# Kernel tuning notes

Measured on AMD Instinct MI355X. Metric: run time of the kernel, lower is better.

## Reference

```python
import jax, jax.numpy as jnp
from jax import lax
import numpy as np
from itertools import permutations, combinations

GRID = (8, 8, 8)  # width, height, depth


def _build_complex(size):
    """Freudenthal (Kuhn) triangulation of the 3D voxel grid.

    Equivalent role to scipy Delaunay on the regular grid (which is degenerate
    anyway): 6 tetrahedra per unit cube, plus all unique faces, edges, verts.
    Returns:
      simp_verts [n,4] int32 : vertex ids of each simplex, padded by repetition
      simp_dim   [n]   int32 : simplex dimension 0..3
      bnd_cof, bnd_face [m] int32 : (cofacet_id, face_id) boundary incidences
    """
    W, H, D = size

    def vid(p):
        return (p[..., 0] * H + p[..., 1]) * D + p[..., 2]

    e = np.eye(3, dtype=np.int64)
    gx, gy, gz = np.meshgrid(np.arange(W - 1), np.arange(H - 1), np.arange(D - 1), indexing="ij")
    base = np.stack([gx, gy, gz], -1).reshape(-1, 3)
    tet_list = []
    for p in permutations(range(3)):
        v0 = base
        v1 = v0 + e[p[0]]
        v2 = v1 + e[p[1]]
        v3 = v2 + e[p[2]]
        tet_list.append(np.stack([vid(v0), vid(v1), vid(v2), vid(v3)], -1))
    tets = np.unique(np.sort(np.concatenate(tet_list, 0), axis=1), axis=0)
    c3 = np.array(list(combinations(range(4), 3)))
    tris = np.unique(tets[:, c3].reshape(-1, 3), axis=0)
    c2 = np.array(list(combinations(range(3), 2)))
    edges = np.unique(tris[:, c2].reshape(-1, 2), axis=0)

    nV = W * H * D
    nE, nT = len(edges), len(tris)
    eid = {tuple(ed): nV + i for i, ed in enumerate(edges)}
    tid = {tuple(tr): nV + nE + i for i, tr in enumerate(tris)}

    bc, bf = [], []
    for i, ed in enumerate(edges):
        j = nV + i
        bc += [j, j]
        bf += [int(ed[0]), int(ed[1])]
    for i, tr in enumerate(tris):
        j = nV + nE + i
        for pair in combinations(tr, 2):
            bc.append(j)
            bf.append(eid[pair])
    for i, te in enumerate(tets):
        j = nV + nE + nT + i
        for tri in combinations(te, 3):
            bc.append(j)
            bf.append(tid[tri])

    vpad = np.repeat(np.arange(nV)[:, None], 4, axis=1)
    epad = np.pad(edges, ((0, 0), (0, 2)), mode="edge")
    tpad = np.pad(tris, ((0, 0), (0, 1)), mode="edge")
    simp_verts = np.concatenate([vpad, epad, tpad, tets], 0).astype(np.int32)
    simp_dim = np.concatenate([
        np.zeros(nV), np.ones(nE), 2 * np.ones(nT), 3 * np.ones(len(tets))
    ]).astype(np.int32)
    return simp_verts, simp_dim, np.asarray(bc, np.int32), np.asarray(bf, np.int32)


def setup_inputs() -> dict:
    key = jax.random.key(0)
    sv, sd, bc, bf = _build_complex(GRID)
    beta = jax.random.normal(key, (GRID[0] * GRID[1] * GRID[2],), dtype=jnp.float32)
    return {
        "beta": beta,
        "simp_verts": jnp.asarray(sv),
        "simp_dim": jnp.asarray(sd),
        "bnd_cof": jnp.asarray(bc),
        "bnd_face": jnp.asarray(bf),
    }


def _toploss(beta, simp_verts, simp_dim, bnd_cof, bnd_face):
    n = simp_dim.shape[0]
    # Superlevel-set (sublevel=False) filtration: simplex value = min over vertices.
    f = jnp.min(beta[simp_verts], axis=1)  # [n]
    # Filtration order: f descending, tie-break dimension ascending.
    perm = jnp.lexsort((simp_dim, lax.stop_gradient(-f)))
    inv = jnp.zeros(n, jnp.int32).at[perm].set(jnp.arange(n, dtype=jnp.int32))
    # Boundary matrix over GF(2), stored row-major: B[j] = boundary of simplex j.
    B = jnp.zeros((n, n), dtype=bool).at[inv[bnd_cof], inv[bnd_face]].set(True)

    idxs = jnp.arange(n, dtype=jnp.int32)
    low = lambda row: jnp.max(jnp.where(row, idxs, -1))

    def body(j, state):
        B, piv = state

        def cond(c):
            return (c[1] >= 0) & (piv[c[1]] >= 0)

        def step(c):
            r = c[0] ^ B[piv[c[1]]]
            return r, low(r)

        row = B[j]
        row, l = lax.while_loop(cond, step, (row, low(row)))
        B = B.at[j].set(row)
        piv2 = piv.at[jnp.maximum(l, 0)].set(jnp.asarray(j, jnp.int32))
        piv = jnp.where(l >= 0, piv2, piv)
        return B, piv

    _, piv = lax.fori_loop(0, n, body, (B, jnp.full((n,), -1, jnp.int32)))
    piv = lax.stop_gradient(piv)  # combinatorial pairing: constant wrt beta

    fs = f[perm]           # filtration values in sorted order (differentiable)
    ds = simp_dim[perm]
    paired = piv >= 0      # simplex i born, killed by simplex piv[i]
    lengths = jnp.where(paired, fs - fs[jnp.maximum(piv, 0)], 0.0)  # birth - death >= 0
    # SumBarcodeLengths(dim=0): all finite dim-0 bars (essential bars have length 0).
    loss0 = jnp.sum(jnp.where(ds == 0, lengths, 0.0))
    # PartialSumBarcodeLengths(dim=1, skip=1): sum of dim-1 lengths minus the largest.
    len1 = jnp.where(ds == 1, lengths, 0.0)
    loss1 = jnp.sum(len1) - jnp.max(len1)
    return loss0 + loss1


_toploss_jit = jax.jit(_toploss)


def reference(beta, simp_verts, simp_dim, bnd_cof, bnd_face):
    return _toploss_jit(beta, simp_verts, simp_dim, bnd_cof, bnd_face)
```

## Files before the change

### kernel.cpp

```cpp
#include <hip/hip_runtime.h>
#include <stdint.h>

#define MAX_E 3072
#define MAX_T 4608
#define MAX_V 1024
#define TW    72
#define INF_I 0x7fffffff
#define RB_E  12
#define RB_T  18
#define RB_C  24
#define TBLK  18

typedef unsigned long long ull;

__device__ int   g_erank[MAX_E];
__device__ int   g_eorder[MAX_E];
__device__ float g_ef[MAX_E];
__device__ int   g_trank[MAX_T];
__device__ float g_tf[MAX_T];
__device__ __attribute__((aligned(16))) ull g_rows[(size_t)MAX_E * TW];
__device__ int   g_mst[MAX_E];
__device__ int   g_clr[MAX_E];
__device__ int   g_ilow[MAX_E];
__device__ float g_loss0;

__device__ __forceinline__ int ub_dim(const int* __restrict__ sd, int nS, int d) {
  int lo = 0, hi = nS;
  while (lo < hi) { int mid = (lo + hi) >> 1; if (sd[mid] <= d) lo = mid + 1; else hi = mid; }
  return lo;
}

__device__ __forceinline__ ull rank_key(float f, int j) {
  unsigned bb = __float_as_uint(f);
  unsigned ord = (bb & 0x80000000u) ? ~bb : (bb | 0x80000000u);
  return ((ull)ord << 32) | (ull)(0xffffffffu - (unsigned)j);
}

__device__ __forceinline__ int rank_count64(const ull* __restrict__ sk, int n, ull ki) {
  int r = 0, j = 0;
  for (; j + 8 <= n; j += 8) {
    ulonglong2 a = *(const ulonglong2*)(sk + j);
    ulonglong2 b = *(const ulonglong2*)(sk + j + 2);
    ulonglong2 c = *(const ulonglong2*)(sk + j + 4);
    ulonglong2 d = *(const ulonglong2*)(sk + j + 6);
    r += (int)(a.x > ki) + (int)(a.y > ki) + (int)(b.x > ki) + (int)(b.y > ki)
       + (int)(c.x > ki) + (int)(c.y > ki) + (int)(d.x > ki) + (int)(d.y > ki);
  }
  for (; j < n; ++j) r += (int)(sk[j] > ki);
  return r;
}

union SharedK1 {
  struct { alignas(16) ull sk[MAX_T]; } rank;
  struct {
    int par[MAX_V]; ull cand[MAX_V]; int hookTo[MAX_V];
    int eu[MAX_E], ev2[MAX_E];
    float efv[MAX_E];
    unsigned int ekey[MAX_E];
    unsigned short alive[2][MAX_E];
    unsigned char mstf[MAX_E];
  } uf;
};

__global__ void __launch_bounds__(256) k_main1(const float* __restrict__ beta,
                                               const int* __restrict__ sv,
                                               const int* __restrict__ sd,
                                               int nV, int nS) {
  __shared__ SharedK1 sh;
  __shared__ float aS[4], aM[4], aW[4];
  __shared__ int nNext, nRoots;
  int b = blockIdx.x, tid = threadIdx.x;
  int nE = ub_dim(sd, nS, 1) - nV;

  if (b < RB_E) {
    int i = b * 256 + tid;
    float fi = 0.f;
    for (int j = tid; j < nE; j += 256) {
      const int* p = &sv[(size_t)(nV + j) * 4];
      float fj = fminf(beta[p[0]], beta[p[1]]);
      if (j == i) fi = fj;
      sh.rank.sk[j] = rank_key(fj, j);
    }
    __syncthreads();
    if (i >= nE) return;
    int r = rank_count64(sh.rank.sk, nE, sh.rank.sk[i]);
    g_erank[i] = r;
    g_eorder[r] = i;
    g_ef[r] = fi;
    return;
  }
  if (b < RB_E + RB_T) {
    int nT = ub_dim(sd, nS, 2) - nV - nE;
    int base = nV + nE;
    int i = (b - RB_E) * 256 + tid;
    float fi = 0.f;
    for (int j = tid; j < nT; j += 256) {
      const int* p = &sv[(size_t)(base + j) * 4];
      float fj = fminf(fminf(beta[p[0]], beta[p[1]]), beta[p[2]]);
      if (j == i) fi = fj;
      sh.rank.sk[j] = rank_key(fj, j);
    }
    __syncthreads();
    if (i >= nT) return;
    int r = rank_count64(sh.rank.sk, nT, sh.rank.sk[i]);
    g_trank[i] = r;
    g_tf[r] = fi;
    return;
  }
  if (b > RB_E + RB_T) {
    size_t i = (size_t)(b - RB_E - RB_T - 1) * 256 + tid;
    size_t stride = (size_t)RB_C * 256;
    for (size_t k = i; k < (size_t)MAX_E * TW; k += stride) g_rows[k] = 0ull;
    for (size_t k = i; k < MAX_E; k += stride) g_ilow[k] = -1;
    return;
  }

  int lane = tid & 63, wave = tid >> 6;
  for (int v = tid; v < nV; v += 256) sh.uf.par[v] = v;
  for (int e = tid; e < nE; e += 256) {
    int u = sv[(size_t)(nV + e) * 4];
    int v = sv[(size_t)(nV + e) * 4 + 1];
    sh.uf.eu[e] = u; sh.uf.ev2[e] = v;
    float fe = fminf(beta[u], beta[v]);
    sh.uf.efv[e] = fe;
    unsigned int bb = __float_as_uint(fe);
    sh.uf.ekey[e] = (bb & 0x80000000u) ? ~bb : (bb | 0x80000000u);
    sh.uf.alive[0][e] = (unsigned short)e;
    sh.uf.mstf[e] = 0;
  }
  float s = 0.f, m = -3.0e38f;
  for (int v = tid; v < nV; v += 256) { float fv = beta[v]; s += fv; m = fmaxf(m, fv); }
  float W = 0.f;
  int nAlive = nE, cur = 0;
  __syncthreads();
  for (int phase = 0; phase < 20 && nAlive > 0; ++phase) {
    for (int v = tid; v < nV; v += 256) sh.uf.cand[v] = 0ull;
    if (tid == 0) { nNext = 0; nRoots = 0; }
    __syncthreads();
    for (int i0 = 0; i0 < nAlive; i0 += 256) {
      int i = i0 + tid;
      int e = -1, ra = 0, rb = 0;
      bool cross = false;
      if (i < nAlive) {
        e = sh.uf.alive[cur][i];
        ra = sh.uf.eu[e];  while (sh.uf.par[ra] != ra) ra = sh.uf.par[ra];
        rb = sh.uf.ev2[e]; while (sh.uf.par[rb] != rb) rb = sh.uf.par[rb];
        cross = (ra != rb);
      }
      ull mb = __ballot(cross);
      int base = 0;
      if (lane == 0 && mb) base = atomicAdd(&nNext, __popcll(mb));
      base = __shfl(base, 0);
      if (cross) {
        int off = __popcll(mb & ((1ull << lane) - 1ull));
        sh.uf.alive[cur ^ 1][base + off] = (unsigned short)e;
        ull key = ((ull)sh.uf.ekey[e] << 32) | (ull)(0xffffffffu - (unsigned)e);
        atomicMax(&sh.uf.cand[ra], key);
        atomicMax(&sh.uf.cand[rb], key);
      }
    }
    __syncthreads();
    for (int v = tid; v < nV; v += 256) {
      int t = -1;
      ull cv = sh.uf.cand[v];
      if (sh.uf.par[v] == v && cv) {
        int e = (int)(0xffffffffu - (unsigned)(cv & 0xffffffffu));
        int ra = sh.uf.eu[e];  while (sh.uf.par[ra] != ra) ra = sh.uf.par[ra];
        int rb = sh.uf.ev2[e]; while (sh.uf.par[rb] != rb) rb = sh.uf.par[rb];
        int other = (ra == v) ? rb : ra;
        if (sh.uf.cand[other] != cv || v < other) t = other;
      }
      sh.uf.hookTo[v] = t;
    }
    __syncthreads();
    for (int v = tid; v < nV; v += 256) {
      int t = sh.uf.hookTo[v];
      if (t >= 0) {
        sh.uf.par[v] = t;
        int e = (int)(0xffffffffu - (unsigned)(sh.uf.cand[v] & 0xffffffffu));
        W += sh.uf.efv[e];
        sh.uf.mstf[e] = 1;
      }
    }
    __syncthreads();
    for (int it = 0; it < 5; ++it) {
      for (int v = tid; v < nV; v += 256) {
        int p = sh.uf.par[v]; int gp = sh.uf.par[p];
        if (p != gp) sh.uf.par[v] = gp;
      }
      __syncthreads();
    }
    int loc = 0;
    for (int v = tid; v < nV; v += 256) loc += (sh.uf.par[v] == v);
    #pragma unroll
    for (int off = 32; off; off >>= 1) loc += __shfl_xor(loc, off, 64);
    if (lane == 0) atomicAdd(&nRoots, loc);
    __syncthreads();
    if (nRoots <= 1) break;
    nAlive = nNext;
    cur ^= 1;
    __syncthreads();
  }
  __syncthreads();
  for (int e = tid; e < nE; e += 256) g_mst[e] = sh.uf.mstf[e];
  #pragma unroll
  for (int off = 32; off; off >>= 1) {
    s += __shfl_xor(s, off, 64);
    m = fmaxf(m, __shfl_xor(m, off, 64));
    W += __shfl_xor(W, off, 64);
  }
  if (lane == 0) { aS[wave] = s; aM[wave] = m; aW[wave] = W; }
  __syncthreads();
  if (tid == 0) {
    float S = 0.f, M = -3.0e38f, WW = 0.f;
    for (int i = 0; i < 4; ++i) { S += aS[i]; M = fmaxf(M, aM[i]); WW += aW[i]; }
    g_loss0 = S - M - WW;
  }
}

__global__ void __launch_bounds__(256) k_scat(const int* __restrict__ bf,
                                              const int* __restrict__ sd,
                                              int nV, int nS) {
  int nE = ub_dim(sd, nS, 1) - nV;
  int tid = threadIdx.x;
  if (blockIdx.x == TBLK) {
    for (int r = tid; r < nE; r += 256)
      g_clr[nE - 1 - r] = g_mst[g_eorder[r]];
    return;
  }
  int nT = ub_dim(sd, nS, 2) - nV - nE;
  int t = blockIdx.x * 256 + tid;
  if (t >= nT) return;
  int lpos = nT - 1 - g_trank[t];
  size_t base = (size_t)2 * nE + (size_t)3 * t;
  ull bit = 1ull << (lpos & 63);
  int word = lpos >> 6;
  for (int j = 0; j < 3; ++j) {
    int e = bf[base + j] - nV;
    int rr = nE - 1 - g_erank[e];
    atomicOr(&g_rows[(size_t)rr * TW + word], bit);
    atomicMax(&g_ilow[rr], lpos);
  }
}

__device__ __forceinline__ int row_low(ull x, ull y, int lane) {
  ull msk = __ballot((x | y) != 0ull);
  int hb = y ? (lane * 128 + 127 - __clzll(y)) : (lane * 128 + 63 - __clzll(x | 1ull));
  return msk ? __shfl(hb, 63 - __clzll(msk)) : -1;
}

__global__ void __launch_bounds__(1024) k_reduce(const int* __restrict__ sd,
                                                 int nV, int nS,
                                                 float* __restrict__ out) {
  __shared__ int spiv[MAX_T];
  __shared__ int lowA[MAX_E];
  __shared__ int stamp[MAX_E];
  __shared__ int lists[2][MAX_E];
  __shared__ int tailq[64];
  __shared__ int cnts[2];
  __shared__ int workIdx;
  __shared__ float ssum[16], smax[16];

  int tid = threadIdx.x;
  int lane = tid & 63;
  int wave = tid >> 6;
  int nE = ub_dim(sd, nS, 1) - nV;
  int nT = ub_dim(sd, nS, 2) - nV - nE;

  for (int i = tid; i < nT; i += 1024) spiv[i] = INF_I;
  for (int r = tid; r < nE; r += 1024) stamp[r] = -1;
  if (tid == 0) { cnts[0] = 0; cnts[1] = 0; }
  __syncthreads();

  for (int r = tid; r < nE; r += 1024) {
    int l = g_clr[r] ? -1 : g_ilow[r];
    lowA[r] = l;
    if (l >= 0) atomicMin(&spiv[l], r);
  }
  __syncthreads();
  for (int r = tid; r < nE; r += 1024) {
    int l = lowA[r];
    if (l >= 0 && spiv[l] != r) { int q = atomicAdd(&cnts[0], 1); lists[0][q] = r; }
  }
  __syncthreads();

  int pass = 0;
  int cnt = cnts[0];
  while (cnt > 0 && pass < 50000) {
    int cur = pass & 1, nxt = cur ^ 1;

    if (cnt <= 8) {
      if (wave == 0) {
        for (int i = lane; i < cnt; i += 64) tailq[i] = lists[cur][i];
        int head = 0, tl = cnt;
        while (head < tl) {
          int r = tailq[head & 63]; head++;
          int l = lowA[r];
          ull wx = 0, wy = 0;
          bool loaded = false;
          for (;;) {
            int p = spiv[l];
            ull px = 0, py = 0;
            if (lane < 36) {
              ulonglong2 v = *(const ulonglong2*)&g_rows[(size_t)p * TW + 2 * lane];
              px = v.x; py = v.y;
            }
            if (!loaded) {
              if (lane < 36) {
                ulonglong2 v = *(const ulonglong2*)&g_rows[(size_t)r * TW + 2 * lane];
                wx = v.x; wy = v.y;
              }
              loaded = true;
            }
            wx ^= px; wy ^= py;
            l = row_low(wx, wy, lane);
            if (l < 0) break;
            int old = 0;
            if (lane == 0) old = atomicMin(&spiv[l], r);
            old = __shfl(old, 0);
            if (old > r) {
              if (lane < 36) {
                ulonglong2 v; v.x = wx; v.y = wy;
                *(ulonglong2*)&g_rows[(size_t)r * TW + 2 * lane] = v;
              }
              if (lane == 0) lowA[r] = l;
              if (old != INF_I) { if (lane == 0) tailq[tl & 63] = old; tl++; }
              break;
            }
          }
        }
      }
      __syncthreads();
      break;
    }

    if (tid == 0) { cnts[nxt] = 0; workIdx = 0; }
    for (int i = tid; i < cnt; i += 1024) stamp[lists[cur][i]] = pass;
    __syncthreads();
    for (;;) {
      int idx = 0;
      if (lane == 0) idx = atomicAdd(&workIdx, 1);
      idx = __shfl(idx, 0);
      if (idx >= cnt) break;
      int r = lists[cur][idx];
      int l = lowA[r];
      ull wx = 0, wy = 0;
      bool loaded = false, modified = false;
      for (;;) {
        int p = spiv[l];
        ull px = 0, py = 0;
        if (lane < 36) {
          ulonglong2 v = *(const ulonglong2*)&g_rows[(size_t)p * TW + 2 * lane];
          px = v.x; py = v.y;
        }
        if (stamp[p] == pass) {
          if (lane == 0) { int q = atomicAdd(&cnts[nxt], 1); lists[nxt][q] = r; }
          break;
        }
        if (!loaded) {
          if (lane < 36) {
            ulonglong2 v = *(const ulonglong2*)&g_rows[(size_t)r * TW + 2 * lane];
            wx = v.x; wy = v.y;
          }
          loaded = true;
        }
        wx ^= px; wy ^= py;
        modified = true;
        l = row_low(wx, wy, lane);
        if (lane == 0) lowA[r] = l;
        if (l < 0) break;
        int old = 0;
        if (lane == 0) old = atomicMin(&spiv[l], r);
        old = __shfl(old, 0);
        if (old > r) {
          if (old != INF_I && lane == 0) { int q = atomicAdd(&cnts[nxt], 1); lists[nxt][q] = old; }
          break;
        }
      }
      if (modified && l >= 0 && lane < 36) {
        ulonglong2 v; v.x = wx; v.y = wy;
        *(ulonglong2*)&g_rows[(size_t)r * TW + 2 * lane] = v;
      }
    }
    __syncthreads();
    cnt = cnts[nxt];
    pass++;
  }

  float sum = 0.f, mx = 0.f;
  for (int l = tid; l < nT; l += 1024) {
    int r = spiv[l];
    if (r != INF_I) {
      float len = g_ef[nE - 1 - r] - g_tf[nT - 1 - l];
      sum += len;
      mx = fmaxf(mx, len);
    }
  }
  #pragma unroll
  for (int off = 32; off; off >>= 1) {
    sum += __shfl_xor(sum, off, 64);
    mx = fmaxf(mx, __shfl_xor(mx, off, 64));
  }
  if (lane == 0) { ssum[wave] = sum; smax[wave] = mx; }
  __syncthreads();
  if (tid == 0) {
    float S = 0.f, M = 0.f;
    for (int i = 0; i < 16; ++i) { S += ssum[i]; M = fmaxf(M, smax[i]); }
    out[0] = g_loss0 + S - M;
  }
}

extern "C" void kernel_launch(void* const* d_in, const int* in_sizes, int n_in,
                              void* d_out, int out_size, void* d_ws, size_t ws_size,
                              hipStream_t stream) {
  const float* beta = (const float*)d_in[0];
  const int*   sv   = (const int*)d_in[1];
  const int*   sd   = (const int*)d_in[2];
  const int*   bf   = (const int*)d_in[4];
  float* out = (float*)d_out;

  int nV = in_sizes[0];
  int nS = in_sizes[2];

  k_main1<<<RB_E + RB_T + 1 + RB_C, 256, 0, stream>>>(beta, sv, sd, nV, nS);
  k_scat<<<TBLK + 1, 256, 0, stream>>>(bf, sd, nV, nS);
  k_reduce<<<1, 1024, 0, stream>>>(sd, nV, nS, out);
}
```

Baseline: 172.4 us.

## Pack pass stamp into pivot entries, add path-halving find, drop root count

The reduction kernel now packs a pass stamp into the low 14 bits of each pivot table entry, so one shared read both gives the pivot row and tells whether it is still being processed this pass. This removes the separate stamp array and its per-pass fill. In the MST kernel, find uses path halving, pointer-jumping drops from 5 to 2 iterations, and the per-phase root-count reduction and its barrier are gone, so the loop ends only when no cross edges remain. Risks: the pass cap drops to 16000 to fit the 14-bit stamp, and row indices shifted left by 14 must fit in an int.

```diff
diff --git a/kernel.cpp b/kernel.cpp
--- a/kernel.cpp
+++ b/kernel.cpp
@@ -10,6 +10,9 @@
 #define RB_T  18
 #define RB_C  24
 #define TBLK  18
+#define EP_BITS  14
+#define EP_MASK  0x3FFF
+#define EP_DONE  0x3FFF
 
 typedef unsigned long long ull;
 
@@ -48,6 +51,16 @@
   }
   for (; j < n; ++j) r += (int)(sk[j] > ki);
   return r;
+}
+
+__device__ __forceinline__ int uf_find(int* par, int x) {
+  for (;;) {
+    int p = par[x];
+    if (p == x) return x;
+    int gp = par[p];
+    if (p != gp) par[x] = gp;
+    x = gp;
+  }
 }
 
 union SharedK1 {
@@ -68,7 +81,7 @@
                                                int nV, int nS) {
   __shared__ SharedK1 sh;
   __shared__ float aS[4], aM[4], aW[4];
-  __shared__ int nNext, nRoots;
+  __shared__ int nNext;
   int b = blockIdx.x, tid = threadIdx.x;
   int nE = ub_dim(sd, nS, 1) - nV;
 
@@ -116,7 +129,8 @@
   }
 
   int lane = tid & 63, wave = tid >> 6;
-  for (int v = tid; v < nV; v += 256) sh.uf.par[v] = v;
+  int* par = sh.uf.par;
+  for (int v = tid; v < nV; v += 256) par[v] = v;
   for (int e = tid; e < nE; e += 256) {
     int u = sv[(size_t)(nV + e) * 4];
     int v = sv[(size_t)(nV + e) * 4 + 1];
@@ -135,16 +149,17 @@
   __syncthreads();
   for (int phase = 0; phase < 20 && nAlive > 0; ++phase) {
     for (int v = tid; v < nV; v += 256) sh.uf.cand[v] = 0ull;
-    if (tid == 0) { nNext = 0; nRoots = 0; }
+    if (tid == 0) nNext = 0;
     __syncthreads();
     for (int i0 = 0; i0 < nAlive; i0 += 256) {
       int i = i0 + tid;
-      int e = -1, ra = 0, rb = 0;
+      int e = -1;
       bool cross = false;
+      int ra = 0, rb = 0;
       if (i < nAlive) {
         e = sh.uf.alive[cur][i];
-        ra = sh.uf.eu[e];  while (sh.uf.par[ra] != ra) ra = sh.uf.par[ra];
-        rb = sh.uf.ev2[e]; while (sh.uf.par[rb] != rb) rb = sh.uf.par[rb];
+        ra = uf_find(par, sh.uf.eu[e]);
+        rb = uf_find(par, sh.uf.ev2[e]);
         cross = (ra != rb);
       }
       ull mb = __ballot(cross);
@@ -163,10 +178,10 @@
     for (int v = tid; v < nV; v += 256) {
       int t = -1;
       ull cv = sh.uf.cand[v];
-      if (sh.uf.par[v] == v && cv) {
+      if (par[v] == v && cv) {
         int e = (int)(0xffffffffu - (unsigned)(cv & 0xffffffffu));
-        int ra = sh.uf.eu[e];  while (sh.uf.par[ra] != ra) ra = sh.uf.par[ra];
-        int rb = sh.uf.ev2[e]; while (sh.uf.par[rb] != rb) rb = sh.uf.par[rb];
+        int ra = uf_find(par, sh.uf.eu[e]);
+        int rb = uf_find(par, sh.uf.ev2[e]);
         int other = (ra == v) ? rb : ra;
         if (sh.uf.cand[other] != cv || v < other) t = other;
       }
@@ -176,27 +191,20 @@
     for (int v = tid; v < nV; v += 256) {
       int t = sh.uf.hookTo[v];
       if (t >= 0) {
-        sh.uf.par[v] = t;
+        par[v] = t;
         int e = (int)(0xffffffffu - (unsigned)(sh.uf.cand[v] & 0xffffffffu));
         W += sh.uf.efv[e];
         sh.uf.mstf[e] = 1;
       }
     }
     __syncthreads();
-    for (int it = 0; it < 5; ++it) {
+    for (int it = 0; it < 2; ++it) {
       for (int v = tid; v < nV; v += 256) {
-        int p = sh.uf.par[v]; int gp = sh.uf.par[p];
-        if (p != gp) sh.uf.par[v] = gp;
+        int p = par[v]; int gp = par[p];
+        if (p != gp) par[v] = gp;
       }
       __syncthreads();
     }
-    int loc = 0;
-    for (int v = tid; v < nV; v += 256) loc += (sh.uf.par[v] == v);
-    #pragma unroll
-    for (int off = 32; off; off >>= 1) loc += __shfl_xor(loc, off, 64);
-    if (lane == 0) atomicAdd(&nRoots, loc);
-    __syncthreads();
-    if (nRoots <= 1) break;
     nAlive = nNext;
     cur ^= 1;
     __syncthreads();
@@ -254,7 +262,6 @@
                                                  float* __restrict__ out) {
   __shared__ int spiv[MAX_T];
   __shared__ int lowA[MAX_E];
-  __shared__ int stamp[MAX_E];
   __shared__ int lists[2][MAX_E];
   __shared__ int tailq[64];
   __shared__ int cnts[2];
@@ -268,25 +275,24 @@
   int nT = ub_dim(sd, nS, 2) - nV - nE;
 
   for (int i = tid; i < nT; i += 1024) spiv[i] = INF_I;
-  for (int r = tid; r < nE; r += 1024) stamp[r] = -1;
   if (tid == 0) { cnts[0] = 0; cnts[1] = 0; }
   __syncthreads();
 
   for (int r = tid; r < nE; r += 1024) {
     int l = g_clr[r] ? -1 : g_ilow[r];
     lowA[r] = l;
-    if (l >= 0) atomicMin(&spiv[l], r);
+    if (l >= 0) atomicMin(&spiv[l], (r << EP_BITS) | EP_DONE);
   }
   __syncthreads();
   for (int r = tid; r < nE; r += 1024) {
     int l = lowA[r];
-    if (l >= 0 && spiv[l] != r) { int q = atomicAdd(&cnts[0], 1); lists[0][q] = r; }
+    if (l >= 0 && (spiv[l] >> EP_BITS) != r) { int q = atomicAdd(&cnts[0], 1); lists[0][q] = r; }
   }
   __syncthreads();
 
   int pass = 0;
   int cnt = cnts[0];
-  while (cnt > 0 && pass < 50000) {
+  while (cnt > 0 && pass < 16000) {
     int cur = pass & 1, nxt = cur ^ 1;
 
     if (cnt <= 8) {
@@ -299,7 +305,7 @@
           ull wx = 0, wy = 0;
           bool loaded = false;
           for (;;) {
-            int p = spiv[l];
+            int p = spiv[l] >> EP_BITS;
             ull px = 0, py = 0;
             if (lane < 36) {
               ulonglong2 v = *(const ulonglong2*)&g_rows[(size_t)p * TW + 2 * lane];
@@ -316,15 +322,15 @@
             l = row_low(wx, wy, lane);
             if (l < 0) break;
             int old = 0;
-            if (lane == 0) old = atomicMin(&spiv[l], r);
+            if (lane == 0) old = atomicMin(&spiv[l], (r << EP_BITS) | EP_DONE);
             old = __shfl(old, 0);
-            if (old > r) {
+            if (old > ((r << EP_BITS) | EP_DONE)) {
               if (lane < 36) {
                 ulonglong2 v; v.x = wx; v.y = wy;
                 *(ulonglong2*)&g_rows[(size_t)r * TW + 2 * lane] = v;
               }
               if (lane == 0) lowA[r] = l;
-              if (old != INF_I) { if (lane == 0) tailq[tl & 63] = old; tl++; }
+              if (old != INF_I) { if (lane == 0) tailq[tl & 63] = old >> EP_BITS; tl++; }
               break;
             }
           }
@@ -335,7 +341,6 @@
     }
 
     if (tid == 0) { cnts[nxt] = 0; workIdx = 0; }
-    for (int i = tid; i < cnt; i += 1024) stamp[lists[cur][i]] = pass;
     __syncthreads();
     for (;;) {
       int idx = 0;
@@ -347,15 +352,16 @@
       ull wx = 0, wy = 0;
       bool loaded = false, modified = false;
       for (;;) {
-        int p = spiv[l];
+        int val = spiv[l];
+        int p = val >> EP_BITS;
+        if ((val & EP_MASK) == pass) {
+          if (lane == 0) { int q = atomicAdd(&cnts[nxt], 1); lists[nxt][q] = r; }
+          break;
+        }
         ull px = 0, py = 0;
         if (lane < 36) {
           ulonglong2 v = *(const ulonglong2*)&g_rows[(size_t)p * TW + 2 * lane];
           px = v.x; py = v.y;
-        }
-        if (stamp[p] == pass) {
-          if (lane == 0) { int q = atomicAdd(&cnts[nxt], 1); lists[nxt][q] = r; }
-          break;
         }
         if (!loaded) {
           if (lane < 36) {
@@ -369,11 +375,12 @@
         l = row_low(wx, wy, lane);
         if (lane == 0) lowA[r] = l;
         if (l < 0) break;
+        int myval = (r << EP_BITS) | pass;
         int old = 0;
-        if (lane == 0) old = atomicMin(&spiv[l], r);
+        if (lane == 0) old = atomicMin(&spiv[l], myval);
         old = __shfl(old, 0);
-        if (old > r) {
-          if (old != INF_I && lane == 0) { int q = atomicAdd(&cnts[nxt], 1); lists[nxt][q] = old; }
+        if (old > myval) {
+          if (old != INF_I && lane == 0) { int q = atomicAdd(&cnts[nxt], 1); lists[nxt][q] = old >> EP_BITS; }
           break;
         }
       }
@@ -389,8 +396,9 @@
 
   float sum = 0.f, mx = 0.f;
   for (int l = tid; l < nT; l += 1024) {
-    int r = spiv[l];
-    if (r != INF_I) {
+    int v = spiv[l];
+    if (v != INF_I) {
+      int r = v >> EP_BITS;
       float len = g_ef[nE - 1 - r] - g_tf[nT - 1 - l];
       sum += len;
       mx = fmaxf(mx, len);
```

New measurement: 172.6 us. About the same (+0.1%).
